# Optimization experiments

Hardware: AMD Instinct MI355X
Metric: run time of the kernel (lower is better)

The kernel has to match this reference:

```python
import jax, jax.numpy as jnp
import numpy as np

IN_FEATURES = 8192
OUT_FEATURES = 8192
MAX_STATES = 100
THRESHOLD = MAX_STATES // 2  # 50


def setup_inputs() -> dict:
    key = jax.random.key(0)
    k1, k2, k3, k4 = jax.random.split(key, 4)
    # mimic module init: states = randn*2 + threshold, clamped to [1, max_states]
    synapse_states = jnp.clip(
        jax.random.normal(k1, (OUT_FEATURES, IN_FEATURES), dtype=jnp.float32) * 2.0 + THRESHOLD,
        1.0, float(MAX_STATES))
    spike_input = (jax.random.uniform(k2, (IN_FEATURES,), dtype=jnp.float32) > 0.5).astype(jnp.float32)
    # non-trivial running state so all update paths are exercised
    membrane_potential = jax.random.uniform(k3, (OUT_FEATURES,), dtype=jnp.float32) * 4.0
    adaptive_threshold = jnp.full((OUT_FEATURES,), 5.0, dtype=jnp.float32)
    eligibility_trace = jax.random.uniform(k4, (OUT_FEATURES, IN_FEATURES), dtype=jnp.float32)
    return {
        "spike_input": spike_input,
        "synapse_states": synapse_states,
        "membrane_potential": membrane_potential,
        "adaptive_threshold": adaptive_threshold,
        "eligibility_trace": eligibility_trace,
    }


def reference(spike_input, synapse_states, membrane_potential, adaptive_threshold, eligibility_trace):
    # ternary (here effectively binary 0/1) weights from integer-like synapse states
    w = (synapse_states > THRESHOLD).astype(jnp.float32)  # [O, I]
    x = spike_input.reshape(-1)                           # [I]
    current = w @ x                                       # [O] (x @ w.T flattened)
    # membrane decay + integrate
    v_mem = membrane_potential * 0.9 + current            # [O]
    spikes = (v_mem >= adaptive_threshold).astype(jnp.float32)
    # eligibility trace: decay + outer-product Hebbian term, clamped
    new_trace = jnp.clip(eligibility_trace * 0.8 + jnp.outer(spikes, x), 0.0, 5.0)
    # homeostatic threshold adaptation
    new_threshold = jnp.clip(adaptive_threshold + (spikes - 0.1) * 0.1, 1.0, 20.0)
    # reset membrane where spiked, leaky retain otherwise
    new_membrane = v_mem * (1.0 - spikes) * 0.1
    return spikes, new_membrane, new_threshold, new_trace
```

## Files before the change

### kernel.cpp

```cpp
#include <hip/hip_runtime.h>


constexpr int O_FEAT = 8192;
constexpr int I_FEAT = 8192;
constexpr float STATE_THR = 50.0f;

typedef float f32x4 __attribute__((ext_vector_type(4)));

__global__ __launch_bounds__(256) void snn_fused_wave(
    const float* __restrict__ x,
    const float* __restrict__ syn,
    const float* __restrict__ mp,
    const float* __restrict__ thr,
    const float* __restrict__ tr,
    float* __restrict__ out)
{
    const int lane = threadIdx.x & 63;
    const int o = (blockIdx.x * blockDim.x + threadIdx.x) >> 6;
    const long long rowoff = (long long)o * I_FEAT;

    const f32x4* __restrict__ x4 = (const f32x4*)x;
    const f32x4* __restrict__ s4 = (const f32x4*)(syn + rowoff);
    const f32x4* __restrict__ t4 = (const f32x4*)(tr + rowoff);
    f32x4* __restrict__ n4 = (f32x4*)(out + 3LL * O_FEAT + rowoff);

    float sum = 0.0f;
#pragma unroll 4
    for (int j = 0; j < 32; ++j) {
        const int idx = j * 64 + lane;
        const f32x4 sv = s4[idx];
        const f32x4 xv = x4[idx];
        sum += (sv.x > STATE_THR) ? xv.x : 0.0f;
        sum += (sv.y > STATE_THR) ? xv.y : 0.0f;
        sum += (sv.z > STATE_THR) ? xv.z : 0.0f;
        sum += (sv.w > STATE_THR) ? xv.w : 0.0f;
    }

#pragma unroll
    for (int off = 1; off < 64; off <<= 1)
        sum += __shfl_xor(sum, off, 64);

    const float v_mem = __fadd_rn(__fmul_rn(mp[o], 0.9f), sum);
    const float th = thr[o];
    const float s = (v_mem >= th) ? 1.0f : 0.0f;
    if (lane == 0) {
        out[o] = s;
        out[O_FEAT + o] = __fmul_rn(__fmul_rn(v_mem, 1.0f - s), 0.1f);
        float nth = __fadd_rn(th, __fmul_rn(s - 0.1f, 0.1f));
        out[2 * O_FEAT + o] = fminf(fmaxf(nth, 1.0f), 20.0f);
    }

#pragma unroll 4
    for (int j = 0; j < 32; ++j) {
        const int idx = j * 64 + lane;
        const f32x4 tv = t4[idx];
        const f32x4 xv = x4[idx];
        f32x4 r;
        r.x = fminf(fmaxf(__fadd_rn(__fmul_rn(tv.x, 0.8f), s * xv.x), 0.0f), 5.0f);
        r.y = fminf(fmaxf(__fadd_rn(__fmul_rn(tv.y, 0.8f), s * xv.y), 0.0f), 5.0f);
        r.z = fminf(fmaxf(__fadd_rn(__fmul_rn(tv.z, 0.8f), s * xv.z), 0.0f), 5.0f);
        r.w = fminf(fmaxf(__fadd_rn(__fmul_rn(tv.w, 0.8f), s * xv.w), 0.0f), 5.0f);
        __builtin_nontemporal_store(r, &n4[idx]);
    }
}

extern "C" void kernel_launch(void* const* d_in, const int* in_sizes, int n_in,
                              void* d_out, int out_size, void* d_ws, size_t ws_size,
                              hipStream_t stream) {
    const float* x   = (const float*)d_in[0];
    const float* syn = (const float*)d_in[1];
    const float* mp  = (const float*)d_in[2];
    const float* th  = (const float*)d_in[3];
    const float* tr  = (const float*)d_in[4];
    float* out = (float*)d_out;

    snn_fused_wave<<<O_FEAT / 4, 256, 0, stream>>>(x, syn, mp, th, tr, out);
}
```

Before: 149.2 us.

## Assign one block per output row and pack spike bits into masks with popcount

Each output row now goes to a full 256-thread block instead of one wavefront, and a shared-memory reduction combines the four per-wave counts. The input spikes and synapse comparisons are packed into 32-bit masks and counted with popcount, so the trace loop reuses the x mask instead of reloading x. The first two trace vectors are prefetched before the reduction barrier to hide some load latency. This assumes x holds only 0 or 1, which the binary input guarantees. It also adds a block barrier and launches four times as many blocks.

```diff
diff --git a/kernel.cpp b/kernel.cpp
--- a/kernel.cpp
+++ b/kernel.cpp
@@ -7,7 +7,7 @@
 
 typedef float f32x4 __attribute__((ext_vector_type(4)));
 
-__global__ __launch_bounds__(256) void snn_fused_wave(
+__global__ __launch_bounds__(256) void snn_fused_v5(
     const float* __restrict__ x,
     const float* __restrict__ syn,
     const float* __restrict__ mp,
@@ -15,8 +15,8 @@
     const float* __restrict__ tr,
     float* __restrict__ out)
 {
-    const int lane = threadIdx.x & 63;
-    const int o = (blockIdx.x * blockDim.x + threadIdx.x) >> 6;
+    const int t = threadIdx.x;
+    const int o = blockIdx.x;
     const long long rowoff = (long long)o * I_FEAT;
 
     const f32x4* __restrict__ x4 = (const f32x4*)x;
@@ -24,42 +24,55 @@
     const f32x4* __restrict__ t4 = (const f32x4*)(tr + rowoff);
     f32x4* __restrict__ n4 = (f32x4*)(out + 3LL * O_FEAT + rowoff);
 
-    float sum = 0.0f;
-#pragma unroll 4
-    for (int j = 0; j < 32; ++j) {
-        const int idx = j * 64 + lane;
+    const float mpv = mp[o];
+    const float th  = thr[o];
+
+    unsigned xmask = 0u, smask = 0u;
+#pragma unroll
+    for (int j = 0; j < 8; ++j) {
+        const int idx = j * 256 + t;
+        const f32x4 xv = x4[idx];
         const f32x4 sv = s4[idx];
-        const f32x4 xv = x4[idx];
-        sum += (sv.x > STATE_THR) ? xv.x : 0.0f;
-        sum += (sv.y > STATE_THR) ? xv.y : 0.0f;
-        sum += (sv.z > STATE_THR) ? xv.z : 0.0f;
-        sum += (sv.w > STATE_THR) ? xv.w : 0.0f;
+        const unsigned xn = (xv.x != 0.0f ? 1u : 0u) | (xv.y != 0.0f ? 2u : 0u)
+                          | (xv.z != 0.0f ? 4u : 0u) | (xv.w != 0.0f ? 8u : 0u);
+        const unsigned sn = (sv.x > STATE_THR ? 1u : 0u) | (sv.y > STATE_THR ? 2u : 0u)
+                          | (sv.z > STATE_THR ? 4u : 0u) | (sv.w > STATE_THR ? 8u : 0u);
+        xmask |= xn << (j * 4);
+        smask |= sn << (j * 4);
     }
+    int cnt = __popc(xmask & smask);
+
+    const f32x4 tp0 = t4[t];
+    const f32x4 tp1 = t4[256 + t];
 
 #pragma unroll
     for (int off = 1; off < 64; off <<= 1)
-        sum += __shfl_xor(sum, off, 64);
+        cnt += __shfl_xor(cnt, off, 64);
 
-    const float v_mem = __fadd_rn(__fmul_rn(mp[o], 0.9f), sum);
-    const float th = thr[o];
+    __shared__ int wsum[4];
+    if ((t & 63) == 0) wsum[t >> 6] = cnt;
+    __syncthreads();
+    const int total = ((wsum[0] + wsum[1]) + wsum[2]) + wsum[3];
+
+    const float v_mem = __fadd_rn(__fmul_rn(mpv, 0.9f), (float)total);
     const float s = (v_mem >= th) ? 1.0f : 0.0f;
-    if (lane == 0) {
+    if (t == 0) {
         out[o] = s;
         out[O_FEAT + o] = __fmul_rn(__fmul_rn(v_mem, 1.0f - s), 0.1f);
         float nth = __fadd_rn(th, __fmul_rn(s - 0.1f, 0.1f));
         out[2 * O_FEAT + o] = fminf(fmaxf(nth, 1.0f), 20.0f);
     }
 
-#pragma unroll 4
-    for (int j = 0; j < 32; ++j) {
-        const int idx = j * 64 + lane;
-        const f32x4 tv = t4[idx];
-        const f32x4 xv = x4[idx];
+#pragma unroll
+    for (int j = 0; j < 8; ++j) {
+        const int idx = j * 256 + t;
+        const f32x4 tv = (j == 0) ? tp0 : (j == 1) ? tp1 : t4[idx];
+        const unsigned mb = xmask >> (j * 4);
         f32x4 r;
-        r.x = fminf(fmaxf(__fadd_rn(__fmul_rn(tv.x, 0.8f), s * xv.x), 0.0f), 5.0f);
-        r.y = fminf(fmaxf(__fadd_rn(__fmul_rn(tv.y, 0.8f), s * xv.y), 0.0f), 5.0f);
-        r.z = fminf(fmaxf(__fadd_rn(__fmul_rn(tv.z, 0.8f), s * xv.z), 0.0f), 5.0f);
-        r.w = fminf(fmaxf(__fadd_rn(__fmul_rn(tv.w, 0.8f), s * xv.w), 0.0f), 5.0f);
+        r.x = fminf(fmaxf(__fadd_rn(__fmul_rn(tv.x, 0.8f), (mb & 1u) ? s : 0.0f), 0.0f), 5.0f);
+        r.y = fminf(fmaxf(__fadd_rn(__fmul_rn(tv.y, 0.8f), (mb & 2u) ? s : 0.0f), 0.0f), 5.0f);
+        r.z = fminf(fmaxf(__fadd_rn(__fmul_rn(tv.z, 0.8f), (mb & 4u) ? s : 0.0f), 0.0f), 5.0f);
+        r.w = fminf(fmaxf(__fadd_rn(__fmul_rn(tv.w, 0.8f), (mb & 8u) ? s : 0.0f), 0.0f), 5.0f);
         __builtin_nontemporal_store(r, &n4[idx]);
     }
 }
@@ -74,5 +87,5 @@
     const float* tr  = (const float*)d_in[4];
     float* out = (float*)d_out;
 
-    snn_fused_wave<<<O_FEAT / 4, 256, 0, stream>>>(x, syn, mp, th, tr, out);
+    snn_fused_v5<<<O_FEAT, 256, 0, stream>>>(x, syn, mp, th, tr, out);
 }
```

Result: faster. 139.1 us (-6.8%).
